# Kernel tuning notes

Measured on AMD Instinct MI355X. Metric: run time of the kernel, lower is better.

Reference implementation:

```python
import jax, jax.numpy as jnp
import numpy as np

N_NODES = 50000
N_EDGES = 800000
EMBED = 128
HEADS = 8
HEAD_DIM = EMBED // HEADS  # 16
HIDDEN = 512
EPS = 1e-5
SLOPE = 0.2  # DGL GATConv default negative_slope


def setup_inputs() -> dict:
    key = jax.random.key(0)
    ks = jax.random.split(key, 16)
    s = 0.05
    return {
        "x": jax.random.normal(ks[0], (N_NODES, EMBED), dtype=jnp.float32),
        "src": jax.random.randint(ks[1], (N_EDGES,), 0, N_NODES),
        "dst": jax.random.randint(ks[2], (N_EDGES,), 0, N_NODES),
        # GATConv params: fc weight stored as [in, out] (i.e. torch weight transposed)
        "W": jax.random.normal(ks[3], (EMBED, HEADS * HEAD_DIM), dtype=jnp.float32) * s,
        "attn_l": jax.random.normal(ks[4], (HEADS, HEAD_DIM), dtype=jnp.float32) * s,
        "attn_r": jax.random.normal(ks[5], (HEADS, HEAD_DIM), dtype=jnp.float32) * s,
        "gat_bias": jnp.zeros((EMBED,), dtype=jnp.float32),
        # BatchNorm1d affine params (training-mode batch stats used in math)
        "gamma1": jnp.ones((EMBED,), dtype=jnp.float32),
        "beta1": jnp.zeros((EMBED,), dtype=jnp.float32),
        "gamma2": jnp.ones((EMBED,), dtype=jnp.float32),
        "beta2": jnp.zeros((EMBED,), dtype=jnp.float32),
        # FFN weights stored as [in, out]
        "W1": jax.random.normal(ks[6], (EMBED, HIDDEN), dtype=jnp.float32) * s,
        "b1": jnp.zeros((HIDDEN,), dtype=jnp.float32),
        "W2": jax.random.normal(ks[7], (HIDDEN, EMBED), dtype=jnp.float32) * s,
        "b2": jnp.zeros((EMBED,), dtype=jnp.float32),
    }


def _batchnorm(y, gamma, beta):
    mu = jnp.mean(y, axis=0)
    var = jnp.var(y, axis=0)  # biased variance, as torch BN uses for normalization
    return gamma * (y - mu) * jax.lax.rsqrt(var + EPS) + beta


def reference(x, src, dst, W, attn_l, attn_r, gat_bias,
              gamma1, beta1, gamma2, beta2, W1, b1, W2, b2):
    N = x.shape[0]
    # ---- GATConv ----
    feat = (x @ W).reshape(N, HEADS, HEAD_DIM)              # [N,H,D]
    el = jnp.sum(feat * attn_l, axis=-1)                    # [N,H]
    er = jnp.sum(feat * attn_r, axis=-1)                    # [N,H]
    e = jax.nn.leaky_relu(el[src] + er[dst], SLOPE)         # [E,H]
    # segment softmax over incoming edges of each dst node
    m = jax.ops.segment_max(e, dst, num_segments=N)         # [N,H] (-inf for empty)
    ex = jnp.exp(e - m[dst])                                # [E,H]
    denom = jax.ops.segment_sum(ex, dst, num_segments=N)    # [N,H]
    a = ex / denom[dst]                                     # [E,H]
    msg = feat[src] * a[:, :, None]                         # [E,H,D]
    rst = jax.ops.segment_sum(msg, dst, num_segments=N)     # [N,H,D]
    rst = rst + gat_bias.reshape(HEADS, HEAD_DIM)
    h = x + rst.reshape(N, EMBED)                           # skip connection
    # ---- FFN block: BN -> skip(MLP) -> BN ----
    h = _batchnorm(h, gamma1, beta1)
    y = jax.nn.relu(h @ W1 + b1) @ W2 + b2
    h = _batchnorm(h + y, gamma2, beta2)
    return h
```

## Files before the change

### kernel.cpp

```cpp
#include <hip/hip_runtime.h>

#define NCH 128
#define NH  8
#define HID 512
#define SLOPE 0.2f
#define BN_EPS 1e-5f
#define LDP 136
#define NPW 2
#define CHUNK 2048

typedef __attribute__((ext_vector_type(8))) short short8;
typedef __attribute__((ext_vector_type(4))) float floatx4;

__device__ inline unsigned short f2bf(float f) {
  unsigned u = __float_as_uint(f);
  u += 0x7fffu + ((u >> 16) & 1u);
  return (unsigned short)(u >> 16);
}
__device__ inline float bflo(unsigned u) { return __uint_as_float(u << 16); }
__device__ inline float bfhi(unsigned u) { return __uint_as_float(u & 0xffff0000u); }

__global__ void prep_all(const float* __restrict__ W, unsigned short* __restrict__ WT,
                         const float* __restrict__ W1, unsigned short* __restrict__ w1f,
                         const float* __restrict__ W2, unsigned short* __restrict__ w2f,
                         float* __restrict__ stats, int* __restrict__ cnt, int N) {
  int b = blockIdx.x, tid = threadIdx.x;
  if (b < 64) {
    int i = b * 256 + tid;
    int n = i >> 7, k = i & 127;
    WT[i] = f2bf(W[k * NCH + n]);
  } else if (b < 320) {
    int i = (b - 64) * 256 + tid;
    int ntile = i >> 11, kk = (i >> 9) & 3, lane = (i >> 3) & 63, j = i & 7;
    int k = kk * 32 + (lane >> 4) * 8 + j;
    int n = ntile * 16 + (lane & 15);
    w1f[i] = f2bf(W1[k * HID + n]);
  } else if (b < 576) {
    int i = (b - 320) * 256 + tid;
    int ch = i >> 14, nt = (i >> 11) & 7, kk = (i >> 9) & 3, lane = (i >> 3) & 63, j = i & 7;
    int k = ch * 128 + kk * 32 + (lane >> 4) * 8 + j;
    int n = nt * 16 + (lane & 15);
    w2f[i] = f2bf(W2[k * NCH + n]);
  } else if (b < 596) {
    int i = (b - 576) * 256 + tid;
    ((float4*)stats)[i] = make_float4(0.f, 0.f, 0.f, 0.f);
  } else {
    int i = (b - 596) * 256 + tid;
    int n4 = (N + 3) >> 2;
    if (i < n4) ((int4*)cnt)[i] = make_int4(0, 0, 0, 0);
  }
}

__global__ __launch_bounds__(256) void feat_hist(const float* __restrict__ x,
                                                 const unsigned short* __restrict__ WT,
                                                 const float* __restrict__ attn_r,
                                                 unsigned short* __restrict__ featb,
                                                 float* __restrict__ er,
                                                 int N,
                                                 const int* __restrict__ dst, int* __restrict__ cnt,
                                                 int E, int FB) {
  __shared__ unsigned short rowX[64 * LDP];
  __shared__ unsigned short wt[128 * LDP];
  __shared__ float arL[128];
  if (blockIdx.x >= FB) {
    int i = (blockIdx.x - FB) * 256 + threadIdx.x;
    if (i < E) atomicAdd(&cnt[dst[i]], 1);
    return;
  }
  int tid = threadIdx.x;
  int r0 = blockIdx.x * 64;
  int lane = tid & 63, wid = tid >> 6;
  int quad = lane >> 4, lc = lane & 15;
  int mrow = (wid & 1) * 32;
  int chalf = (wid >> 1) * 64;

  if (tid < 128) arL[tid] = attn_r[tid];
  {
    int n = tid >> 1, kg = (tid & 1) * 64;
    const uint4* g = (const uint4*)(WT + n * NCH + kg);
    uint4* l = (uint4*)&wt[n * LDP + kg];
    for (int i = 0; i < 8; i++) l[i] = g[i];
  }
  {
    int r = tid >> 2, kg = (tid & 3) * 32;
    int gr = r0 + r;
    unsigned short tmp[32];
    if (gr < N) {
      const float4* gp = (const float4*)(x + (size_t)gr * NCH + kg);
      for (int i = 0; i < 8; i++) {
        float4 v = gp[i];
        tmp[i * 4 + 0] = f2bf(v.x); tmp[i * 4 + 1] = f2bf(v.y);
        tmp[i * 4 + 2] = f2bf(v.z); tmp[i * 4 + 3] = f2bf(v.w);
      }
    } else {
      for (int i = 0; i < 32; i++) tmp[i] = 0;
    }
    uint4* l = (uint4*)&rowX[r * LDP + kg];
    const uint4* s = (const uint4*)tmp;
    for (int i = 0; i < 4; i++) l[i] = s[i];
  }
  __syncthreads();

  floatx4 acc[2][4];
  for (int rt = 0; rt < 2; rt++) for (int tt = 0; tt < 4; tt++) acc[rt][tt] = (floatx4)(0.f);
  for (int kk = 0; kk < 4; kk++) {
    short8 a0 = *(const short8*)&rowX[(mrow + lc) * LDP + kk * 32 + quad * 8];
    short8 a1 = *(const short8*)&rowX[(mrow + 16 + lc) * LDP + kk * 32 + quad * 8];
    for (int tt = 0; tt < 4; tt++) {
      short8 b = *(const short8*)&wt[(chalf + tt * 16 + lc) * LDP + kk * 32 + quad * 8];
      acc[0][tt] = __builtin_amdgcn_mfma_f32_16x16x32_bf16(a0, b, acc[0][tt], 0, 0, 0);
      acc[1][tt] = __builtin_amdgcn_mfma_f32_16x16x32_bf16(a1, b, acc[1][tt], 0, 0, 0);
    }
  }
  __syncthreads();
  for (int rt = 0; rt < 2; rt++)
    for (int tt = 0; tt < 4; tt++)
      for (int r = 0; r < 4; r++)
        rowX[(mrow + rt * 16 + quad * 4 + r) * LDP + chalf + tt * 16 + lc] = f2bf(acc[rt][tt][r]);
  __syncthreads();
  {
    int r = tid >> 2, kg = (tid & 3) * 32;
    int gr = r0 + r;
    if (gr < N) {
      uint4* gp = (uint4*)(featb + (size_t)gr * NCH + kg);
      const uint4* l = (const uint4*)&rowX[r * LDP + kg];
      for (int i = 0; i < 4; i++) gp[i] = l[i];
    }
  }
  for (int p = tid; p < 512; p += 256) {
    int row = p >> 3, h = p & 7;
    int gr = r0 + row;
    if (gr < N) {
      const unsigned* rp = (const unsigned*)&rowX[row * LDP + h * 16];
      float sr = 0.f;
      for (int q = 0; q < 8; q++) {
        unsigned u = rp[q];
        int c = h * 16 + 2 * q;
        sr += bflo(u) * arL[c] + bfhi(u) * arL[c + 1];
      }
      er[gr * NH + h] = sr;
    }
  }
}

__global__ void scan_part(const int* __restrict__ cnt, int* __restrict__ off,
                          int* __restrict__ bsum, int N) {
  __shared__ int sh[256];
  int t = threadIdx.x, i = blockIdx.x * 256 + t;
  int v = (i < N) ? cnt[i] : 0;
  sh[t] = v; __syncthreads();
  for (int d = 1; d < 256; d <<= 1) {
    int u = (t >= d) ? sh[t - d] : 0;
    __syncthreads();
    sh[t] += u;
    __syncthreads();
  }
  if (i < N) off[i] = sh[t] - v;
  if (t == 255) bsum[blockIdx.x] = sh[255];
}

__global__ void scan_add2(int* __restrict__ off, const int* __restrict__ bsum,
                          int* __restrict__ bktcur, int N, int nb) {
  __shared__ int sh[256];
  int t = threadIdx.x;
  int v = (t < nb) ? bsum[t] : 0;
  sh[t] = v; __syncthreads();
  for (int d = 1; d < 256; d <<= 1) {
    int u = (t >= d) ? sh[t - d] : 0;
    __syncthreads();
    sh[t] += u;
    __syncthreads();
  }
  int pref = (blockIdx.x > 0) ? sh[blockIdx.x - 1] : 0;
  int i = blockIdx.x * 256 + t;
  if (i < N) {
    int w = off[i] + pref;
    off[i] = w;
    if (t == 0) bktcur[blockIdx.x] = w;
  }
}

__global__ __launch_bounds__(256) void bin_scatter(const int* __restrict__ src,
                                                   const int* __restrict__ dst,
                                                   int* __restrict__ bktcur,
                                                   uint2* __restrict__ ebuf, int E) {
  __shared__ int bc[256];
  __shared__ int bbase[256];
  int tid = threadIdx.x;
  int s = blockIdx.x * CHUNK;
  int e = min(s + CHUNK, E);
  bc[tid] = 0;
  __syncthreads();
  for (int i = s + tid; i < e; i += 256) atomicAdd(&bc[dst[i] >> 8], 1);
  __syncthreads();
  int c = bc[tid];
  if (c > 0) bbase[tid] = atomicAdd(&bktcur[tid], c);
  __syncthreads();
  bc[tid] = 0;
  __syncthreads();
  for (int i = s + tid; i < e; i += 256) {
    int d = dst[i];
    int b = d >> 8;
    int r = atomicAdd(&bc[b], 1);
    ebuf[bbase[b] + r] = make_uint2((unsigned)src[i], (unsigned)d);
  }
}

__global__ __launch_bounds__(256) void final_scatter(const uint2* __restrict__ ebuf,
                                                     const int* __restrict__ off,
                                                     int* __restrict__ ssrc,
                                                     int E, int N, int NBK) {
  __shared__ int lcur[256];
  __shared__ int sbeg, send;
  int tid = threadIdx.x;
  int b = blockIdx.x;
  int n0 = b * 256;
  int node = n0 + tid;
  lcur[tid] = (node < N) ? off[node] : 0;
  if (tid == 0) {
    sbeg = off[n0];
    send = (b == NBK - 1) ? E : off[n0 + 256];
  }
  __syncthreads();
  int beg = sbeg, end = send;
  for (int i = beg + tid; i < end; i += 256) {
    uint2 ed = ebuf[i];
    int r = atomicAdd(&lcur[(int)ed.y - n0], 1);
    ssrc[r] = (int)ed.x;
  }
}

__global__ __launch_bounds__(256) void gat_gather7(const int* __restrict__ ssrc,
                                                   const int* __restrict__ off,
                                                   const int* __restrict__ cnt,
                                                   const float* __restrict__ attn_l,
                                                   const float* __restrict__ er,
                                                   const unsigned short* __restrict__ featb,
                                                   const float* __restrict__ x,
                                                   const float* __restrict__ gatb,
                                                   float* __restrict__ hbuf,
                                                   float* __restrict__ stats, int N) {
  __shared__ float ps[4][128], pq[4][128];
  int tid = threadIdx.x;
  int lane = tid & 63, w = tid >> 6;
  int hme = lane >> 3;
  int c0 = 2 * lane;
  float2 al2 = *(const float2*)(attn_l + c0);
  float alx = al2.x, aly = al2.y;
  float gb0 = gatb[c0], gb1 = gatb[c0 + 1];
  float s0 = 0.f, s1 = 0.f, q0 = 0.f, q1 = 0.f;
  int base = blockIdx.x * (4 * NPW) + w * NPW;
  for (int j = 0; j < NPW; j++) {
    int node = base + j;
    if (node >= N) break;
    node = __builtin_amdgcn_readfirstlane(node);
    float erh = er[node * NH + hme];
    int beg = __builtin_amdgcn_readfirstlane(off[node]);
    int num = __builtin_amdgcn_readfirstlane(cnt[node]);
    const int* sp = ssrc + beg;
    float acc0 = 0.f, acc1 = 0.f, den = 0.f;
    int i = 0;
    for (; i + 8 <= num; i += 8) {
      int n0 = __builtin_amdgcn_readfirstlane(sp[i + 0]);
      int n1 = __builtin_amdgcn_readfirstlane(sp[i + 1]);
      int n2 = __builtin_amdgcn_readfirstlane(sp[i + 2]);
      int n3 = __builtin_amdgcn_readfirstlane(sp[i + 3]);
      int n4 = __builtin_amdgcn_readfirstlane(sp[i + 4]);
      int n5 = __builtin_amdgcn_readfirstlane(sp[i + 5]);
      int n6 = __builtin_amdgcn_readfirstlane(sp[i + 6]);
      int n7 = __builtin_amdgcn_readfirstlane(sp[i + 7]);
      unsigned f0 = ((const unsigned*)(featb + (size_t)n0 * NCH))[lane];
      unsigned f1 = ((const unsigned*)(featb + (size_t)n1 * NCH))[lane];
      unsigned f2 = ((const unsigned*)(featb + (size_t)n2 * NCH))[lane];
      unsigned f3 = ((const unsigned*)(featb + (size_t)n3 * NCH))[lane];
      unsigned f4 = ((const unsigned*)(featb + (size_t)n4 * NCH))[lane];
      unsigned f5 = ((const unsigned*)(featb + (size_t)n5 * NCH))[lane];
      unsigned f6 = ((const unsigned*)(featb + (size_t)n6 * NCH))[lane];
      unsigned f7 = ((const unsigned*)(featb + (size_t)n7 * NCH))[lane];
      float p0 = bflo(f0) * alx + bfhi(f0) * aly;
      float p1 = bflo(f1) * alx + bfhi(f1) * aly;
      float p2 = bflo(f2) * alx + bfhi(f2) * aly;
      float p3 = bflo(f3) * alx + bfhi(f3) * aly;
      float p4 = bflo(f4) * alx + bfhi(f4) * aly;
      float p5 = bflo(f5) * alx + bfhi(f5) * aly;
      float p6 = bflo(f6) * alx + bfhi(f6) * aly;
      float p7 = bflo(f7) * alx + bfhi(f7) * aly;
      p0 += __shfl_xor(p0, 1); p1 += __shfl_xor(p1, 1);
      p2 += __shfl_xor(p2, 1); p3 += __shfl_xor(p3, 1);
      p4 += __shfl_xor(p4, 1); p5 += __shfl_xor(p5, 1);
      p6 += __shfl_xor(p6, 1); p7 += __shfl_xor(p7, 1);
      p0 += __shfl_xor(p0, 2); p1 += __shfl_xor(p1, 2);
      p2 += __shfl_xor(p2, 2); p3 += __shfl_xor(p3, 2);
      p4 += __shfl_xor(p4, 2); p5 += __shfl_xor(p5, 2);
      p6 += __shfl_xor(p6, 2); p7 += __shfl_xor(p7, 2);
      p0 += __shfl_xor(p0, 4); p1 += __shfl_xor(p1, 4);
      p2 += __shfl_xor(p2, 4); p3 += __shfl_xor(p3, 4);
      p4 += __shfl_xor(p4, 4); p5 += __shfl_xor(p5, 4);
      p6 += __shfl_xor(p6, 4); p7 += __shfl_xor(p7, 4);
      float e0 = p0 + erh, e1 = p1 + erh, e2 = p2 + erh, e3 = p3 + erh;
      float e4 = p4 + erh, e5 = p5 + erh, e6 = p6 + erh, e7 = p7 + erh;
      e0 = e0 > 0.f ? e0 : SLOPE * e0;  e1 = e1 > 0.f ? e1 : SLOPE * e1;
      e2 = e2 > 0.f ? e2 : SLOPE * e2;  e3 = e3 > 0.f ? e3 : SLOPE * e3;
      e4 = e4 > 0.f ? e4 : SLOPE * e4;  e5 = e5 > 0.f ? e5 : SLOPE * e5;
      e6 = e6 > 0.f ? e6 : SLOPE * e6;  e7 = e7 > 0.f ? e7 : SLOPE * e7;
      float w0 = __expf(e0), w1 = __expf(e1), w2 = __expf(e2), w3 = __expf(e3);
      float w4 = __expf(e4), w5 = __expf(e5), w6 = __expf(e6), w7 = __expf(e7);
      acc0 += w0 * bflo(f0) + w1 * bflo(f1) + w2 * bflo(f2) + w3 * bflo(f3)
            + w4 * bflo(f4) + w5 * bflo(f5) + w6 * bflo(f6) + w7 * bflo(f7);
      acc1 += w0 * bfhi(f0) + w1 * bfhi(f1) + w2 * bfhi(f2) + w3 * bfhi(f3)
            + w4 * bfhi(f4) + w5 * bfhi(f5) + w6 * bfhi(f6) + w7 * bfhi(f7);
      den  += w0 + w1 + w2 + w3 + w4 + w5 + w6 + w7;
    }
    for (; i < num; i++) {
      int s = __builtin_amdgcn_readfirstlane(sp[i]);
      unsigned f = ((const unsigned*)(featb + (size_t)s * NCH))[lane];
      float p = bflo(f) * alx + bfhi(f) * aly;
      p += __shfl_xor(p, 1); p += __shfl_xor(p, 2); p += __shfl_xor(p, 4);
      float e = p + erh;
      e = e > 0.f ? e : SLOPE * e;
      float wv = __expf(e);
      acc0 += wv * bflo(f); acc1 += wv * bfhi(f); den += wv;
    }
    float inv = den > 0.f ? 1.f / den : 0.f;
    float2 xv = *(const float2*)(x + (size_t)node * NCH + c0);
    float h0 = xv.x + acc0 * inv + gb0;
    float h1 = xv.y + acc1 * inv + gb1;
    *(float2*)(hbuf + (size_t)node * NCH + c0) = make_float2(h0, h1);
    s0 += h0; s1 += h1; q0 += h0 * h0; q1 += h1 * h1;
  }
  ps[w][c0] = s0; ps[w][c0 + 1] = s1;
  pq[w][c0] = q0; pq[w][c0 + 1] = q1;
  __syncthreads();
  if (tid < 128) {
    float ss = ps[0][tid] + ps[1][tid] + ps[2][tid] + ps[3][tid];
    float qq = pq[0][tid] + pq[1][tid] + pq[2][tid] + pq[3][tid];
    int rep = blockIdx.x & 7;
    atomicAdd(&stats[rep * 128 + tid], ss);
    atomicAdd(&stats[1024 + rep * 128 + tid], qq);
  }
}

__global__ __launch_bounds__(512, 4) void ffn_mfma2(const float* __restrict__ hbuf,
                                                    const float* __restrict__ g1, const float* __restrict__ be1,
                                                    const unsigned short* __restrict__ w1f,
                                                    const unsigned short* __restrict__ w2f,
                                                    const float* __restrict__ b1, const float* __restrict__ b2,
                                                    float* __restrict__ t, float* __restrict__ stats, int N) {
  __shared__ unsigned short w1t[16384];
  __shared__ unsigned short w2t[16384];
  __shared__ unsigned short scr[8][512];
  __shared__ float b1L[512];
  __shared__ float psc[128], psh[128], b2L[128], csum[128], csq[128];
  int tid = threadIdx.x;
  int lane = tid & 63, wid = tid >> 6;
  int quad = lane >> 4, lc = lane & 15;
  int r0 = blockIdx.x * 128;

  b1L[tid] = b1[tid];
  if (tid < 128) {
    float s = 0.f, sq = 0.f;
    for (int r = 0; r < 8; r++) {
      s  += stats[r * 128 + tid];
      sq += stats[1024 + r * 128 + tid];
    }
    float m = s / (float)N;
    float v = sq / (float)N - m * m;
    float rsv = rsqrtf(v + BN_EPS);
    float scv = g1[tid] * rsv;
    psc[tid] = scv;
    psh[tid] = be1[tid] - scv * m;
    b2L[tid] = b2[tid];
    csum[tid] = 0.f; csq[tid] = 0.f;
  }

  int arow = r0 + wid * 16 + lc;
  float4 av[4][2];
  for (int kk = 0; kk < 4; kk++) {
    if (arow < N) {
      const float4* p = (const float4*)(hbuf + (size_t)arow * NCH + kk * 32 + quad * 8);
      av[kk][0] = p[0]; av[kk][1] = p[1];
    } else {
      av[kk][0] = make_float4(0.f, 0.f, 0.f, 0.f);
      av[kk][1] = make_float4(0.f, 0.f, 0.f, 0.f);
    }
  }
  __syncthreads();

  short8 rowA[4];
  for (int kk = 0; kk < 4; kk++) {
    int c = kk * 32 + quad * 8;
    float4 s0 = *(float4*)&psc[c], s1 = *(float4*)&psc[c + 4];
    float4 h0 = *(float4*)&psh[c], h1 = *(float4*)&psh[c + 4];
    short8 r;
    r[0] = (short)f2bf(av[kk][0].x * s0.x + h0.x);
    r[1] = (short)f2bf(av[kk][0].y * s0.y + h0.y);
    r[2] = (short)f2bf(av[kk][0].z * s0.z + h0.z);
    r[3] = (short)f2bf(av[kk][0].w * s0.w + h0.w);
    r[4] = (short)f2bf(av[kk][1].x * s1.x + h1.x);
    r[5] = (short)f2bf(av[kk][1].y * s1.y + h1.y);
    r[6] = (short)f2bf(av[kk][1].z * s1.z + h1.z);
    r[7] = (short)f2bf(av[kk][1].w * s1.w + h1.w);
    rowA[kk] = r;
  }

  floatx4 acc2[8];
  for (int nt = 0; nt < 8; nt++) acc2[nt] = (floatx4)(0.f);

  for (int ch = 0; ch < 4; ch++) {
    __syncthreads();
    {
      const uint4* g1p = (const uint4*)(w1f + ch * 16384);
      const uint4* g2p = (const uint4*)(w2f + ch * 16384);
      uint4* l1 = (uint4*)w1t;
      uint4* l2 = (uint4*)w2t;
      for (int r = 0; r < 4; r++) {
        l1[tid + r * 512] = g1p[tid + r * 512];
        l2[tid + r * 512] = g2p[tid + r * 512];
      }
    }
    __syncthreads();

    for (int kk = 0; kk < 4; kk++) {
      floatx4 d0 = (floatx4)(0.f), d1 = (floatx4)(0.f);
      int t0 = 2 * kk, t1 = 2 * kk + 1;
      for (int kp = 0; kp < 4; kp++) {
        short8 a0 = *(const short8*)&w1t[(t0 * 4 + kp) * 512 + lane * 8];
        short8 a1 = *(const short8*)&w1t[(t1 * 4 + kp) * 512 + lane * 8];
        d0 = __builtin_amdgcn_mfma_f32_16x16x32_bf16(a0, rowA[kp], d0, 0, 0, 0);
        d1 = __builtin_amdgcn_mfma_f32_16x16x32_bf16(a1, rowA[kp], d1, 0, 0, 0);
      }
      {
        int bi0 = ch * 128 + t0 * 16 + 4 * quad;
        float4 bv0 = *(float4*)&b1L[bi0];
        float4 bv1 = *(float4*)&b1L[bi0 + 16];
        float v0, v1, v2, v3;
        unsigned lo, hi;
        int sidx;
        v0 = fmaxf(d0[0] + bv0.x, 0.f); v1 = fmaxf(d0[1] + bv0.y, 0.f);
        v2 = fmaxf(d0[2] + bv0.z, 0.f); v3 = fmaxf(d0[3] + bv0.w, 0.f);
        lo = (unsigned)f2bf(v0) | ((unsigned)f2bf(v1) << 16);
        hi = (unsigned)f2bf(v2) | ((unsigned)f2bf(v3) << 16);
        sidx = ((quad >> 1) * 16 + lc) * 8 + 4 * (quad & 1);
        *(uint2*)&scr[wid][sidx] = make_uint2(lo, hi);
        v0 = fmaxf(d1[0] + bv1.x, 0.f); v1 = fmaxf(d1[1] + bv1.y, 0.f);
        v2 = fmaxf(d1[2] + bv1.z, 0.f); v3 = fmaxf(d1[3] + bv1.w, 0.f);
        lo = (unsigned)f2bf(v0) | ((unsigned)f2bf(v1) << 16);
        hi = (unsigned)f2bf(v2) | ((unsigned)f2bf(v3) << 16);
        sidx = ((2 + (quad >> 1)) * 16 + lc) * 8 + 4 * (quad & 1);
        *(uint2*)&scr[wid][sidx] = make_uint2(lo, hi);
      }
      short8 a2 = *(const short8*)&scr[wid][lane * 8];
      for (int nt = 0; nt < 8; nt++) {
        short8 bfr = *(const short8*)&w2t[(nt * 4 + kk) * 512 + lane * 8];
        acc2[nt] = __builtin_amdgcn_mfma_f32_16x16x32_bf16(a2, bfr, acc2[nt], 0, 0, 0);
      }
    }
  }

  __syncthreads();
  {
    unsigned short* stash = w1t;
    for (int kk = 0; kk < 4; kk++)
      *(short8*)&stash[wid * 2048 + lc * 128 + kk * 32 + quad * 8] = rowA[kk];
  }
  __syncthreads();

  for (int nt = 0; nt < 8; nt++) {
    int col = nt * 16 + lc;
    float b2v = b2L[col];
    float s = 0.f, q = 0.f;
    for (int reg = 0; reg < 4; reg++) {
      int grow = r0 + wid * 16 + quad * 4 + reg;
      if (grow < N) {
        float base = bflo((unsigned)w1t[wid * 2048 + (quad * 4 + reg) * 128 + col]);
        float tv = base + acc2[nt][reg] + b2v;
        t[(size_t)grow * NCH + col] = tv;
        s += tv; q += tv * tv;
      }
    }
    s += __shfl_xor(s, 16); s += __shfl_xor(s, 32);
    q += __shfl_xor(q, 16); q += __shfl_xor(q, 32);
    if (quad == 0) { atomicAdd(&csum[col], s); atomicAdd(&csq[col], q); }
  }
  __syncthreads();
  if (tid < 128) {
    atomicAdd(&stats[16384 + tid * 16], csum[tid]);
    atomicAdd(&stats[18432 + tid * 16], csq[tid]);
  }
}

__global__ __launch_bounds__(256) void bn2_apply2(const float* __restrict__ t,
                                                  const float* __restrict__ g, const float* __restrict__ b,
                                                  const float* __restrict__ stats,
                                                  float* __restrict__ out, int N) {
  __shared__ float scs[128], shs[128];
  int tid = threadIdx.x;
  if (tid < 128) {
    float s = stats[16384 + tid * 16], sq = stats[18432 + tid * 16];
    float m = s / (float)N;
    float v = sq / (float)N - m * m;
    float rsv = rsqrtf(v + BN_EPS);
    float gg = g[tid] * rsv;
    scs[tid] = gg;
    shs[tid] = b[tid] - gg * m;
  }
  __syncthreads();
  int i = blockIdx.x * 256 + tid;
  int tot4 = N * 32;
  if (i < tot4) {
    float4 v = ((const float4*)t)[i];
    int c = (i & 31) * 4;
    float4 o;
    o.x = v.x * scs[c + 0] + shs[c + 0];
    o.y = v.y * scs[c + 1] + shs[c + 1];
    o.z = v.z * scs[c + 2] + shs[c + 2];
    o.w = v.w * scs[c + 3] + shs[c + 3];
    ((float4*)out)[i] = o;
  }
}

extern "C" void kernel_launch(void* const* d_in, const int* in_sizes, int n_in,
                              void* d_out, int out_size, void* d_ws, size_t ws_size,
                              hipStream_t stream) {
  const float* x       = (const float*)d_in[0];
  const int*   src     = (const int*)d_in[1];
  const int*   dst     = (const int*)d_in[2];
  const float* W       = (const float*)d_in[3];
  const float* attn_l  = (const float*)d_in[4];
  const float* attn_r  = (const float*)d_in[5];
  const float* gatb    = (const float*)d_in[6];
  const float* gamma1  = (const float*)d_in[7];
  const float* beta1   = (const float*)d_in[8];
  const float* gamma2  = (const float*)d_in[9];
  const float* beta2   = (const float*)d_in[10];
  const float* W1      = (const float*)d_in[11];
  const float* b1      = (const float*)d_in[12];
  const float* W2      = (const float*)d_in[13];
  const float* b2      = (const float*)d_in[14];
  float* out = (float*)d_out;

  const int N = in_sizes[0] / NCH;
  const int E = in_sizes[1];
  const int nb = (N + 255) / 256;
  const int EB = (E + 255) / 256;
  const int FB = (N + 63) / 64;
  const int BB = (E + CHUNK - 1) / CHUNK;

  float* hbuf  = (float*)d_ws;
  float* t     = hbuf + (size_t)N * NCH;
  float* er    = t + (size_t)N * NCH;
  float* stats = er + (size_t)N * NH;
  unsigned short* featb = (unsigned short*)(stats + 20480);
  unsigned short* WT    = featb + (size_t)N * NCH;
  unsigned short* w1f   = WT + NCH * NCH;
  unsigned short* w2f   = w1f + HID * NCH;
  int* cnt    = (int*)(w2f + HID * NCH);
  int* off    = cnt + N;
  int* bktcur = off + N;
  int* bsum   = bktcur + 256;
  int* ssrc   = bsum + 256;
  uint2* ebuf = (uint2*)(ssrc + E);

  const int cb = (((N + 3) / 4) + 255) / 256;
  prep_all<<<596 + cb, 256, 0, stream>>>(W, WT, W1, w1f, W2, w2f, stats, cnt, N);

  feat_hist<<<FB + EB, 256, 0, stream>>>(x, WT, attn_r, featb, er, N, dst, cnt, E, FB);

  scan_part<<<nb, 256, 0, stream>>>(cnt, off, bsum, N);
  scan_add2<<<nb, 256, 0, stream>>>(off, bsum, bktcur, N, nb);

  bin_scatter<<<BB, 256, 0, stream>>>(src, dst, bktcur, ebuf, E);
  final_scatter<<<nb, 256, 0, stream>>>(ebuf, off, ssrc, E, N, nb);

  gat_gather7<<<(N + 4 * NPW - 1) / (4 * NPW), 256, 0, stream>>>(ssrc, off, cnt, attn_l, er,
                                                                 featb, x, gatb, hbuf, stats, N);

  ffn_mfma2<<<(N + 127) / 128, 512, 0, stream>>>(hbuf, gamma1, beta1,
                                                 w1f, w2f, b1, b2, t, stats, N);

  bn2_apply2<<<(N * 32 + 255) / 256, 256, 0, stream>>>(t, gamma2, beta2, stats, out, N);
}
```

Baseline: 269.3 us.

## Shrink FFN block to 64 rows and halve weight-staging LDS chunks

The FFN kernel now uses 256-thread blocks that each handle 64 rows. It streams W1/W2 in eight half-size chunks through a single 32KB LDS buffer instead of four 64KB chunks, which lowers LDS per block and should let more blocks share a CU. In exchange each block reloads the weights twice as often and there are twice as many barriers. The second BN statistics move from strided per-channel atomics to eight replicated slots that are summed in bn2_apply, which cuts atomic contention, and the stats zeroing shrinks to match.

```diff
diff --git a/kernel.cpp b/kernel.cpp
--- a/kernel.cpp
+++ b/kernel.cpp
@@ -41,11 +41,11 @@
     int k = ch * 128 + kk * 32 + (lane >> 4) * 8 + j;
     int n = nt * 16 + (lane & 15);
     w2f[i] = f2bf(W2[k * NCH + n]);
-  } else if (b < 596) {
+  } else if (b < 580) {
     int i = (b - 576) * 256 + tid;
     ((float4*)stats)[i] = make_float4(0.f, 0.f, 0.f, 0.f);
   } else {
-    int i = (b - 596) * 256 + tid;
+    int i = (b - 580) * 256 + tid;
     int n4 = (N + 3) >> 2;
     if (i < n4) ((int4*)cnt)[i] = make_int4(0, 0, 0, 0);
   }
@@ -340,23 +340,25 @@
   }
 }
 
-__global__ __launch_bounds__(512, 4) void ffn_mfma2(const float* __restrict__ hbuf,
+__global__ __launch_bounds__(256, 4) void ffn_mfma3(const float* __restrict__ hbuf,
                                                     const float* __restrict__ g1, const float* __restrict__ be1,
                                                     const unsigned short* __restrict__ w1f,
                                                     const unsigned short* __restrict__ w2f,
                                                     const float* __restrict__ b1, const float* __restrict__ b2,
                                                     float* __restrict__ t, float* __restrict__ stats, int N) {
-  __shared__ unsigned short w1t[16384];
-  __shared__ unsigned short w2t[16384];
-  __shared__ unsigned short scr[8][512];
+  __shared__ unsigned short wbuf[16384];
+  __shared__ unsigned short scr[4][512];
   __shared__ float b1L[512];
   __shared__ float psc[128], psh[128], b2L[128], csum[128], csq[128];
+  unsigned short* w1t = wbuf;
+  unsigned short* w2t = wbuf + 8192;
   int tid = threadIdx.x;
   int lane = tid & 63, wid = tid >> 6;
   int quad = lane >> 4, lc = lane & 15;
-  int r0 = blockIdx.x * 128;
+  int r0 = blockIdx.x * 64;
 
   b1L[tid] = b1[tid];
+  b1L[tid + 256] = b1[tid + 256];
   if (tid < 128) {
     float s = 0.f, sq = 0.f;
     for (int r = 0; r < 8; r++) {
@@ -406,31 +408,35 @@
   floatx4 acc2[8];
   for (int nt = 0; nt < 8; nt++) acc2[nt] = (floatx4)(0.f);
 
-  for (int ch = 0; ch < 4; ch++) {
+  for (int ch2 = 0; ch2 < 8; ch2++) {
+    int ch = ch2 >> 1, kb = 2 * (ch2 & 1);
     __syncthreads();
     {
-      const uint4* g1p = (const uint4*)(w1f + ch * 16384);
-      const uint4* g2p = (const uint4*)(w2f + ch * 16384);
+      const uint4* g1p = (const uint4*)(w1f + ch2 * 8192);
       uint4* l1 = (uint4*)w1t;
       uint4* l2 = (uint4*)w2t;
+      const uint4* g2f4 = (const uint4*)w2f;
       for (int r = 0; r < 4; r++) {
-        l1[tid + r * 512] = g1p[tid + r * 512];
-        l2[tid + r * 512] = g2p[tid + r * 512];
+        int qq = tid + r * 256;
+        l1[qq] = g1p[qq];
+        int run = qq >> 6, rem4 = qq & 63;
+        int nt = run >> 1, kkl = run & 1;
+        l2[qq] = g2f4[((ch * 8 + nt) * 4 + kb + kkl) * 64 + rem4];
       }
     }
     __syncthreads();
 
-    for (int kk = 0; kk < 4; kk++) {
+    for (int kk2 = 0; kk2 < 2; kk2++) {
       floatx4 d0 = (floatx4)(0.f), d1 = (floatx4)(0.f);
-      int t0 = 2 * kk, t1 = 2 * kk + 1;
+      int t0loc = 2 * kk2, t1loc = 2 * kk2 + 1;
       for (int kp = 0; kp < 4; kp++) {
-        short8 a0 = *(const short8*)&w1t[(t0 * 4 + kp) * 512 + lane * 8];
-        short8 a1 = *(const short8*)&w1t[(t1 * 4 + kp) * 512 + lane * 8];
+        short8 a0 = *(const short8*)&w1t[(t0loc * 4 + kp) * 512 + lane * 8];
+        short8 a1 = *(const short8*)&w1t[(t1loc * 4 + kp) * 512 + lane * 8];
         d0 = __builtin_amdgcn_mfma_f32_16x16x32_bf16(a0, rowA[kp], d0, 0, 0, 0);
         d1 = __builtin_amdgcn_mfma_f32_16x16x32_bf16(a1, rowA[kp], d1, 0, 0, 0);
       }
       {
-        int bi0 = ch * 128 + t0 * 16 + 4 * quad;
+        int bi0 = ch2 * 64 + t0loc * 16 + 4 * quad;
         float4 bv0 = *(float4*)&b1L[bi0];
         float4 bv1 = *(float4*)&b1L[bi0 + 16];
         float v0, v1, v2, v3;
@@ -451,7 +457,7 @@
       }
       short8 a2 = *(const short8*)&scr[wid][lane * 8];
       for (int nt = 0; nt < 8; nt++) {
-        short8 bfr = *(const short8*)&w2t[(nt * 4 + kk) * 512 + lane * 8];
+        short8 bfr = *(const short8*)&w2t[(nt * 2 + kk2) * 512 + lane * 8];
         acc2[nt] = __builtin_amdgcn_mfma_f32_16x16x32_bf16(a2, bfr, acc2[nt], 0, 0, 0);
       }
     }
@@ -459,9 +465,8 @@
 
   __syncthreads();
   {
-    unsigned short* stash = w1t;
     for (int kk = 0; kk < 4; kk++)
-      *(short8*)&stash[wid * 2048 + lc * 128 + kk * 32 + quad * 8] = rowA[kk];
+      *(short8*)&wbuf[wid * 2048 + lc * 128 + kk * 32 + quad * 8] = rowA[kk];
   }
   __syncthreads();
 
@@ -472,7 +477,7 @@
     for (int reg = 0; reg < 4; reg++) {
       int grow = r0 + wid * 16 + quad * 4 + reg;
       if (grow < N) {
-        float base = bflo((unsigned)w1t[wid * 2048 + (quad * 4 + reg) * 128 + col]);
+        float base = bflo((unsigned)wbuf[wid * 2048 + (quad * 4 + reg) * 128 + col]);
         float tv = base + acc2[nt][reg] + b2v;
         t[(size_t)grow * NCH + col] = tv;
         s += tv; q += tv * tv;
@@ -484,8 +489,9 @@
   }
   __syncthreads();
   if (tid < 128) {
-    atomicAdd(&stats[16384 + tid * 16], csum[tid]);
-    atomicAdd(&stats[18432 + tid * 16], csq[tid]);
+    int rep = blockIdx.x & 7;
+    atomicAdd(&stats[2048 + rep * 128 + tid], csum[tid]);
+    atomicAdd(&stats[3072 + rep * 128 + tid], csq[tid]);
   }
 }
 
@@ -496,7 +502,11 @@
   __shared__ float scs[128], shs[128];
   int tid = threadIdx.x;
   if (tid < 128) {
-    float s = stats[16384 + tid * 16], sq = stats[18432 + tid * 16];
+    float s = 0.f, sq = 0.f;
+    for (int r = 0; r < 8; r++) {
+      s  += stats[2048 + r * 128 + tid];
+      sq += stats[3072 + r * 128 + tid];
+    }
     float m = s / (float)N;
     float v = sq / (float)N - m * m;
     float rsv = rsqrtf(v + BN_EPS);
@@ -562,7 +572,7 @@
   uint2* ebuf = (uint2*)(ssrc + E);
 
   const int cb = (((N + 3) / 4) + 255) / 256;
-  prep_all<<<596 + cb, 256, 0, stream>>>(W, WT, W1, w1f, W2, w2f, stats, cnt, N);
+  prep_all<<<580 + cb, 256, 0, stream>>>(W, WT, W1, w1f, W2, w2f, stats, cnt, N);
 
   feat_hist<<<FB + EB, 256, 0, stream>>>(x, WT, attn_r, featb, er, N, dst, cnt, E, FB);
 
@@ -575,8 +585,8 @@
   gat_gather7<<<(N + 4 * NPW - 1) / (4 * NPW), 256, 0, stream>>>(ssrc, off, cnt, attn_l, er,
                                                                  featb, x, gatb, hbuf, stats, N);
 
-  ffn_mfma2<<<(N + 127) / 128, 512, 0, stream>>>(hbuf, gamma1, beta1,
-                                                 w1f, w2f, b1, b2, t, stats, N);
+  ffn_mfma3<<<(N + 63) / 64, 256, 0, stream>>>(hbuf, gamma1, beta1,
+                                               w1f, w2f, b1, b2, t, stats, N);
 
   bn2_apply2<<<(N * 32 + 255) / 256, 256, 0, stream>>>(t, gamma2, beta2, stats, out, N);
 }
```

Measured after the change: 297.7 us. 10.5% more time.

## Read FFN weight fragments directly from global memory instead of LDS staging

Applied to the files above, without the earlier changes.

The FFN MFMA kernel no longer stages W1/W2 chunks into shared memory with block barriers. Each lane instead loads its pre-swizzled bf16 fragments straight from global memory, relying on L1/L2 caching since every block reads the same weights. The row stash is written once up front, which removes the final barriers, and launch bounds drop to 3 blocks per SM. This frees LDS and removes the per-chunk syncs, but it exposes MFMAs to global load latency and raises L2 traffic.

```diff
diff --git a/kernel.cpp b/kernel.cpp
--- a/kernel.cpp
+++ b/kernel.cpp
@@ -340,14 +340,13 @@
   }
 }
 
-__global__ __launch_bounds__(512, 4) void ffn_mfma2(const float* __restrict__ hbuf,
+__global__ __launch_bounds__(512, 3) void ffn_mfma4(const float* __restrict__ hbuf,
                                                     const float* __restrict__ g1, const float* __restrict__ be1,
                                                     const unsigned short* __restrict__ w1f,
                                                     const unsigned short* __restrict__ w2f,
                                                     const float* __restrict__ b1, const float* __restrict__ b2,
                                                     float* __restrict__ t, float* __restrict__ stats, int N) {
-  __shared__ unsigned short w1t[16384];
-  __shared__ unsigned short w2t[16384];
+  __shared__ unsigned short stash[16384];
   __shared__ unsigned short scr[8][512];
   __shared__ float b1L[512];
   __shared__ float psc[128], psh[128], b2L[128], csum[128], csq[128];
@@ -403,34 +402,27 @@
     rowA[kk] = r;
   }
 
+  for (int kk = 0; kk < 4; kk++)
+    *(short8*)&stash[wid * 2048 + lc * 128 + kk * 32 + quad * 8] = rowA[kk];
+
   floatx4 acc2[8];
   for (int nt = 0; nt < 8; nt++) acc2[nt] = (floatx4)(0.f);
 
+  const unsigned short* w1p = w1f + lane * 8;
+  const unsigned short* w2p = w2f + lane * 8;
+
   for (int ch = 0; ch < 4; ch++) {
-    __syncthreads();
-    {
-      const uint4* g1p = (const uint4*)(w1f + ch * 16384);
-      const uint4* g2p = (const uint4*)(w2f + ch * 16384);
-      uint4* l1 = (uint4*)w1t;
-      uint4* l2 = (uint4*)w2t;
-      for (int r = 0; r < 4; r++) {
-        l1[tid + r * 512] = g1p[tid + r * 512];
-        l2[tid + r * 512] = g2p[tid + r * 512];
-      }
-    }
-    __syncthreads();
-
     for (int kk = 0; kk < 4; kk++) {
       floatx4 d0 = (floatx4)(0.f), d1 = (floatx4)(0.f);
-      int t0 = 2 * kk, t1 = 2 * kk + 1;
+      int t0 = ch * 8 + 2 * kk, t1 = t0 + 1;
       for (int kp = 0; kp < 4; kp++) {
-        short8 a0 = *(const short8*)&w1t[(t0 * 4 + kp) * 512 + lane * 8];
-        short8 a1 = *(const short8*)&w1t[(t1 * 4 + kp) * 512 + lane * 8];
+        short8 a0 = *(const short8*)(w1p + (size_t)(t0 * 4 + kp) * 512);
+        short8 a1 = *(const short8*)(w1p + (size_t)(t1 * 4 + kp) * 512);
         d0 = __builtin_amdgcn_mfma_f32_16x16x32_bf16(a0, rowA[kp], d0, 0, 0, 0);
         d1 = __builtin_amdgcn_mfma_f32_16x16x32_bf16(a1, rowA[kp], d1, 0, 0, 0);
       }
       {
-        int bi0 = ch * 128 + t0 * 16 + 4 * quad;
+        int bi0 = ch * 128 + 2 * kk * 16 + 4 * quad;
         float4 bv0 = *(float4*)&b1L[bi0];
         float4 bv1 = *(float4*)&b1L[bi0 + 16];
         float v0, v1, v2, v3;
@@ -451,19 +443,11 @@
       }
       short8 a2 = *(const short8*)&scr[wid][lane * 8];
       for (int nt = 0; nt < 8; nt++) {
-        short8 bfr = *(const short8*)&w2t[(nt * 4 + kk) * 512 + lane * 8];
+        short8 bfr = *(const short8*)(w2p + (size_t)(((ch * 8 + nt) * 4 + kk)) * 512);
         acc2[nt] = __builtin_amdgcn_mfma_f32_16x16x32_bf16(a2, bfr, acc2[nt], 0, 0, 0);
       }
     }
   }
-
-  __syncthreads();
-  {
-    unsigned short* stash = w1t;
-    for (int kk = 0; kk < 4; kk++)
-      *(short8*)&stash[wid * 2048 + lc * 128 + kk * 32 + quad * 8] = rowA[kk];
-  }
-  __syncthreads();
 
   for (int nt = 0; nt < 8; nt++) {
     int col = nt * 16 + lc;
@@ -472,7 +456,7 @@
     for (int reg = 0; reg < 4; reg++) {
       int grow = r0 + wid * 16 + quad * 4 + reg;
       if (grow < N) {
-        float base = bflo((unsigned)w1t[wid * 2048 + (quad * 4 + reg) * 128 + col]);
+        float base = bflo((unsigned)stash[wid * 2048 + (quad * 4 + reg) * 128 + col]);
         float tv = base + acc2[nt][reg] + b2v;
         t[(size_t)grow * NCH + col] = tv;
         s += tv; q += tv * tv;
@@ -575,7 +559,7 @@
   gat_gather7<<<(N + 4 * NPW - 1) / (4 * NPW), 256, 0, stream>>>(ssrc, off, cnt, attn_l, er,
                                                                  featb, x, gatb, hbuf, stats, N);
 
-  ffn_mfma2<<<(N + 127) / 128, 512, 0, stream>>>(hbuf, gamma1, beta1,
+  ffn_mfma4<<<(N + 127) / 128, 512, 0, stream>>>(hbuf, gamma1, beta1,
                                                  w1f, w2f, b1, b2, t, stats, N);
 
   bn2_apply2<<<(N * 32 + 255) / 256, 256, 0, stream>>>(t, gamma2, beta2, stats, out, N);
```

Result: slower. 296.3 us (+10.0%).
